# Kernel optimization log

Hardware: AMD Instinct MI355X
Metric: run time of the kernel (lower is better)

Reference implementation:

```python
import jax, jax.numpy as jnp
import numpy as np

N_HEADS = 16
WINDOW_SIZE = 128


def setup_inputs() -> dict:
    key = jax.random.key(0)
    ks = jax.random.split(key, 5)
    B, T, D = 2, 2048, 1024
    x = jax.random.normal(ks[0], (B, T, D), dtype=jnp.float32)
    w_qkv = jax.random.normal(ks[1], (3 * D, D), dtype=jnp.float32) * (D ** -0.5)
    b_qkv = jax.random.normal(ks[2], (3 * D,), dtype=jnp.float32) * 0.01
    w_out = jax.random.normal(ks[3], (D, D), dtype=jnp.float32) * (D ** -0.5)
    b_out = jax.random.normal(ks[4], (D,), dtype=jnp.float32) * 0.01
    return {"x": x, "w_qkv": w_qkv, "b_qkv": b_qkv, "w_out": w_out, "b_out": b_out}


def reference(x, w_qkv, b_qkv, w_out, b_out):
    B, T, D = x.shape
    H = N_HEADS
    hd = D // H
    scale = hd ** -0.5

    # qkv projection: (B,T,3D) -> (3,B,H,T,hd)
    qkv = (x @ w_qkv.T + b_qkv).reshape(B, T, 3, H, hd)
    qkv = jnp.transpose(qkv, (2, 0, 3, 1, 4))
    q, k, v = qkv[0], qkv[1], qkv[2]

    pos = jnp.arange(T)
    # mask[i, j]: |j - i| <= w/2 and j >= i  (faithful to original, which
    # due to its index orientation allows query i to attend to keys j >= i)
    mask = (jnp.abs(pos[None, :] - pos[:, None]) <= WINDOW_SIZE // 2) & (
        pos[None, :] >= pos[:, None]
    )

    attn = jnp.einsum("bhqd,bhkd->bhqk", q, k) * scale  # (B,H,T,T)
    attn = jnp.where(mask[None, None], attn, -jnp.inf)
    attn = jax.nn.softmax(attn, axis=-1)
    attn = jnp.nan_to_num(attn, nan=0.0)

    out = jnp.einsum("bhqk,bhkd->bhqd", attn, v)  # (B,H,T,hd)
    out = jnp.transpose(out, (0, 2, 1, 3)).reshape(B, T, D)
    return out @ w_out.T + b_out
```

## Files before the change

### kernel.cpp

```cpp
#include <hip/hip_runtime.h>
#include <hip/hip_bf16.h>
#include <stdint.h>


typedef short bf16x8 __attribute__((ext_vector_type(8)));
typedef float f32x4 __attribute__((ext_vector_type(4)));

typedef const __attribute__((address_space(1))) void* gptr_t;
typedef __attribute__((address_space(3))) void* lptr_t;

__device__ __forceinline__ float bf2f(short u) {
    union { float f; uint32_t i; } x;
    x.i = ((uint32_t)(uint16_t)u) << 16;
    return x.f;
}
__device__ __forceinline__ short f2bf(float f) {
    __hip_bfloat16 h = __float2bfloat16(f);
    return *reinterpret_cast<short*>(&h);
}

__global__ __launch_bounds__(256)
void convert_all(const float* __restrict__ x, const float* __restrict__ wq,
                 const float* __restrict__ bq, const float* __restrict__ wo,
                 const float* __restrict__ bo,
                 short* __restrict__ xb, short* __restrict__ wqb, short* __restrict__ bqb,
                 short* __restrict__ wob, short* __restrict__ bob) {
    int i = blockIdx.x * 256 + threadIdx.x;
    const float* src; short* dst; int o;
    if      (i <  524288) { src = x;  dst = xb;  o = i; }
    else if (i <  917504) { src = wq; dst = wqb; o = i - 524288; }
    else if (i <  917888) { src = bq; dst = bqb; o = i - 917504; }
    else if (i < 1048960) { src = wo; dst = wob; o = i - 917888; }
    else if (i < 1049088) { src = bo; dst = bob; o = i - 1048960; }
    else return;
    const int e = o * 8;
    float4 a = *(const float4*)(src + e);
    float4 b = *(const float4*)(src + e + 4);
    short t[8];
    t[0] = f2bf(a.x); t[1] = f2bf(a.y); t[2] = f2bf(a.z); t[3] = f2bf(a.w);
    t[4] = f2bf(b.x); t[5] = f2bf(b.y); t[6] = f2bf(b.z); t[7] = f2bf(b.w);
    *(uint4*)(dst + e) = *(const uint4*)t;
}

__global__ __launch_bounds__(256)
void gemm_bt_128(const short* __restrict__ A, const short* __restrict__ Bt,
                 const short* __restrict__ bias, short* __restrict__ C,
                 int M, int N, int K) {
    __shared__ short As[128 * 32];
    __shared__ short Bs[128 * 32];

    const int tid  = threadIdx.x;
    const int lane = tid & 63;
    const int w    = tid >> 6;
    const int qd   = lane >> 4;
    const int l16  = lane & 15;
    const int wm   = w >> 1;
    const int wn   = w & 1;
    const int mBase = blockIdx.y * 128;
    const int nBase = blockIdx.x * 128;

    f32x4 acc[4][4] = {};

    const int nK = K >> 5;
    for (int kt = 0; kt < nK; ++kt) {
        const int kb = kt << 5;
#pragma unroll
        for (int i = 0; i < 2; ++i) {
            const int e   = i * 2048 + tid * 8;
            const int row = e >> 5;
            const int col = e & 31;
            const short* ga = A  + (size_t)(mBase + row) * K + kb + col;
            const short* gb = Bt + (size_t)(nBase + row) * K + kb + col;
            lptr_t la = (lptr_t)(As + i * 2048 + w * 512);
            lptr_t lb = (lptr_t)(Bs + i * 2048 + w * 512);
            __builtin_amdgcn_global_load_lds((gptr_t)ga, la, 16, 0, 0);
            __builtin_amdgcn_global_load_lds((gptr_t)gb, lb, 16, 0, 0);
        }
        __syncthreads();

        bf16x8 af[4], bfr[4];
#pragma unroll
        for (int mi = 0; mi < 4; ++mi)
            af[mi] = *(const bf16x8*)(As + (wm * 64 + mi * 16 + l16) * 32 + qd * 8);
#pragma unroll
        for (int ni = 0; ni < 4; ++ni)
            bfr[ni] = *(const bf16x8*)(Bs + (wn * 64 + ni * 16 + l16) * 32 + qd * 8);
#pragma unroll
        for (int mi = 0; mi < 4; ++mi)
#pragma unroll
            for (int ni = 0; ni < 4; ++ni)
                acc[mi][ni] = __builtin_amdgcn_mfma_f32_16x16x32_bf16(
                    bfr[ni], af[mi], acc[mi][ni], 0, 0, 0);
        __syncthreads();
    }

#pragma unroll
    for (int ni = 0; ni < 4; ++ni) {
        const int n0 = nBase + wn * 64 + ni * 16 + qd * 4;
        float bv[4];
#pragma unroll
        for (int r = 0; r < 4; ++r) bv[r] = bf2f(bias[n0 + r]);
#pragma unroll
        for (int mi = 0; mi < 4; ++mi) {
            const int m = mBase + wm * 64 + mi * 16 + l16;
            short t[4];
#pragma unroll
            for (int r = 0; r < 4; ++r) t[r] = f2bf(acc[mi][ni][r] + bv[r]);
            *(uint2*)&C[(size_t)m * N + n0] = *(const uint2*)t;
        }
    }
}

__global__ __launch_bounds__(256)
void gemm_bt_64(const short* __restrict__ A, const short* __restrict__ Bt,
                const short* __restrict__ bias, float* __restrict__ C,
                int M, int N, int K) {
    __shared__ short As[64 * 32];
    __shared__ short Bs[128 * 32];

    const int tid  = threadIdx.x;
    const int lane = tid & 63;
    const int w    = tid >> 6;
    const int qd   = lane >> 4;
    const int l16  = lane & 15;
    const int wm   = w >> 1;
    const int wn   = w & 1;
    const int mBase = blockIdx.y * 64;
    const int nBase = blockIdx.x * 128;

    f32x4 acc[2][4] = {};

    const int nK = K >> 5;
    for (int kt = 0; kt < nK; ++kt) {
        const int kb = kt << 5;
        {
            const int e   = tid * 8;
            const int row = e >> 5;
            const int col = e & 31;
            const short* ga = A + (size_t)(mBase + row) * K + kb + col;
            lptr_t la = (lptr_t)(As + w * 512);
            __builtin_amdgcn_global_load_lds((gptr_t)ga, la, 16, 0, 0);
        }
#pragma unroll
        for (int i = 0; i < 2; ++i) {
            const int e   = i * 2048 + tid * 8;
            const int row = e >> 5;
            const int col = e & 31;
            const short* gb = Bt + (size_t)(nBase + row) * K + kb + col;
            lptr_t lb = (lptr_t)(Bs + i * 2048 + w * 512);
            __builtin_amdgcn_global_load_lds((gptr_t)gb, lb, 16, 0, 0);
        }
        __syncthreads();

        bf16x8 af[2], bfr[4];
#pragma unroll
        for (int mi = 0; mi < 2; ++mi)
            af[mi] = *(const bf16x8*)(As + (wm * 32 + mi * 16 + l16) * 32 + qd * 8);
#pragma unroll
        for (int ni = 0; ni < 4; ++ni)
            bfr[ni] = *(const bf16x8*)(Bs + (wn * 64 + ni * 16 + l16) * 32 + qd * 8);
#pragma unroll
        for (int mi = 0; mi < 2; ++mi)
#pragma unroll
            for (int ni = 0; ni < 4; ++ni)
                acc[mi][ni] = __builtin_amdgcn_mfma_f32_16x16x32_bf16(
                    bfr[ni], af[mi], acc[mi][ni], 0, 0, 0);
        __syncthreads();
    }

#pragma unroll
    for (int ni = 0; ni < 4; ++ni) {
        const int n0 = nBase + wn * 64 + ni * 16 + qd * 4;
        float bv[4];
#pragma unroll
        for (int r = 0; r < 4; ++r) bv[r] = bf2f(bias[n0 + r]);
#pragma unroll
        for (int mi = 0; mi < 2; ++mi) {
            const int m = mBase + wm * 32 + mi * 16 + l16;
            f32x4 o;
#pragma unroll
            for (int r = 0; r < 4; ++r) o[r] = acc[mi][ni][r] + bv[r];
            *(f32x4*)&C[(size_t)m * N + n0] = o;
        }
    }
}

__global__ __launch_bounds__(256)
void attn_mfma(const short* __restrict__ qkv, short* __restrict__ attn_out, int B, int T) {
    __shared__ short k_s[128 * 72];
    __shared__ short v_s[144 * 66];
    __shared__ short p_s[64 * 104];

    const int tid  = threadIdx.x;
    const int lane = tid & 63;
    const int w    = tid >> 6;
    const int qd   = lane >> 4;
    const int l16  = lane & 15;
    const int qs   = blockIdx.x * 64;
    const int h    = blockIdx.y;
    const int b    = blockIdx.z;
    const size_t rs   = 3072;
    const size_t base = (size_t)b * T * rs;
    const int qoff = h * 64, koff = 1024 + h * 64, voff = 2048 + h * 64;

#pragma unroll
    for (int i = 0; i < 5; ++i) {
        const int c   = tid + i * 256;
        const int row = c >> 3;
        if (row >= 144) break;
        const int ch = (c & 7) * 8;
        int gr = qs + row; if (gr > T - 1) gr = T - 1;
        uint4 uv = *(const uint4*)(qkv + base + (size_t)gr * rs + voff + ch);
        if (row < 128) {
            uint4 uk = *(const uint4*)(qkv + base + (size_t)gr * rs + koff + ch);
            *(uint4*)&k_s[row * 72 + ch] = uk;
        }
        const uint32_t* vp = (const uint32_t*)&uv;
        uint32_t* vd = (uint32_t*)&v_s[row * 66 + ch];
        vd[0] = vp[0]; vd[1] = vp[1]; vd[2] = vp[2]; vd[3] = vp[3];
    }
    __syncthreads();

    bf16x8 aq0, aq1;
    {
        const short* g = qkv + base + (size_t)(qs + 16 * w + l16) * rs + qoff + qd * 8;
        aq0 = *(const bf16x8*)(g);
        aq1 = *(const bf16x8*)(g + 32);
    }

    f32x4 sacc[5] = {};
#pragma unroll
    for (int u = 0; u < 5; ++u) {
        const int krow = 16 * (w + u) + l16;
        bf16x8 bk0 = *(const bf16x8*)&k_s[krow * 72 + qd * 8];
        bf16x8 bk1 = *(const bf16x8*)&k_s[krow * 72 + 32 + qd * 8];
        sacc[u] = __builtin_amdgcn_mfma_f32_16x16x32_bf16(aq0, bk0, sacc[u], 0, 0, 0);
        sacc[u] = __builtin_amdgcn_mfma_f32_16x16x32_bf16(aq1, bk1, sacc[u], 0, 0, 0);
    }

    const float scale = 0.125f;
    float pw[5][4];
    float inv[4];
#pragma unroll
    for (int r = 0; r < 4; ++r) {
        const int m = 4 * qd + r;
        float mx = -3.4e38f;
#pragma unroll
        for (int u = 0; u < 5; ++u) {
            const int rel = 16 * u + l16 - m;
            const int j   = qs + 16 * (w + u) + l16;
            const bool ok = (rel >= 0) & (rel <= 64) & (j < T);
            const float v = ok ? sacc[u][r] * scale : -3.4e38f;
            pw[u][r] = v;
            mx = fmaxf(mx, v);
        }
#pragma unroll
        for (int msk = 1; msk <= 8; msk <<= 1) mx = fmaxf(mx, __shfl_xor(mx, msk));
        float sum = 0.f;
#pragma unroll
        for (int u = 0; u < 5; ++u) {
            float e = (pw[u][r] <= -3.0e38f) ? 0.f : __expf(pw[u][r] - mx);
            pw[u][r] = e;
            sum += e;
        }
#pragma unroll
        for (int msk = 1; msk <= 8; msk <<= 1) sum += __shfl_xor(sum, msk);
        inv[r] = 1.0f / sum;
    }

#pragma unroll
    for (int u = 0; u < 5; ++u)
#pragma unroll
        for (int r = 0; r < 4; ++r)
            p_s[(16 * w + 4 * qd + r) * 104 + 16 * u + l16] = f2bf(pw[u][r] * inv[r]);
#pragma unroll
    for (int r = 0; r < 4; ++r)
        p_s[(16 * w + 4 * qd + r) * 104 + 80 + l16] = 0;

    f32x4 oacc[4] = {};
#pragma unroll
    for (int ks = 0; ks < 3; ++ks) {
        bf16x8 ap = *(const bf16x8*)&p_s[(16 * w + l16) * 104 + ks * 32 + qd * 8];
#pragma unroll
        for (int dt = 0; dt < 4; ++dt) {
            short t[8];
#pragma unroll
            for (int j = 0; j < 8; ++j)
                t[j] = v_s[(16 * w + ks * 32 + qd * 8 + j) * 66 + 16 * dt + l16];
            bf16x8 bv = *(const bf16x8*)t;
            oacc[dt] = __builtin_amdgcn_mfma_f32_16x16x32_bf16(bv, ap, oacc[dt], 0, 0, 0);
        }
    }

    const size_t row = (size_t)(b * T + qs + 16 * w + l16);
#pragma unroll
    for (int dt = 0; dt < 4; ++dt) {
        short t[4];
#pragma unroll
        for (int r = 0; r < 4; ++r) t[r] = f2bf(oacc[dt][r]);
        *(uint2*)&attn_out[row * 1024 + h * 64 + dt * 16 + qd * 4] = *(const uint2*)t;
    }
}

extern "C" void kernel_launch(void* const* d_in, const int* in_sizes, int n_in,
                              void* d_out, int out_size, void* d_ws, size_t ws_size,
                              hipStream_t stream) {
    (void)in_sizes; (void)n_in; (void)out_size; (void)ws_size;
    const int B = 2, T = 2048, D = 1024;
    const int M = B * T;

    char* ws = (char*)d_ws;
    size_t off = 0;
    short* xb   = (short*)(ws + off); off += (size_t)M * D * 2;
    short* wqkb = (short*)(ws + off); off += (size_t)3 * D * D * 2;
    short* bqkb = (short*)(ws + off); off += (size_t)3 * D * 2;
    short* wob  = (short*)(ws + off); off += (size_t)D * D * 2;
    short* bob  = (short*)(ws + off); off += (size_t)D * 2;
    short* qkv  = (short*)(ws + off); off += (size_t)M * 3 * D * 2;
    short* attn = (short*)(ws + off); off += (size_t)M * D * 2;

    convert_all<<<dim3(4099), 256, 0, stream>>>(
        (const float*)d_in[0], (const float*)d_in[1], (const float*)d_in[2],
        (const float*)d_in[3], (const float*)d_in[4], xb, wqkb, bqkb, wob, bob);

    gemm_bt_128<<<dim3(3 * D / 128, M / 128), 256, 0, stream>>>(
        xb, wqkb, bqkb, qkv, M, 3 * D, D);
    attn_mfma<<<dim3(T / 64, 16, B), 256, 0, stream>>>(qkv, attn, B, T);
    gemm_bt_64<<<dim3(D / 128, M / 64), 256, 0, stream>>>(
        attn, wob, bob, (float*)d_out, M, D, D);
}
```

Baseline: 164.5 us.

## Split-K output projection with a separate bias-reduce kernel and transposed MFMA epilogues

The output projection GEMM now splits K into two halves across blockIdx.z. Each half writes fp32 partials into workspace reused from the dead xb/qkv buffers, and a new reduce kernel adds the two partials plus the fp32 bias. The intent is to double the block count so the GPU is better filled. Both GEMMs also swap MFMA operand order, so the epilogue stores scalar elements with columns contiguous across lanes instead of vector stores. The cost is extra global traffic for the partials, one more kernel launch, and narrower stores.

```diff
diff --git a/kernel.cpp b/kernel.cpp
--- a/kernel.cpp
+++ b/kernel.cpp
@@ -43,9 +43,9 @@
 }
 
 __global__ __launch_bounds__(256)
-void gemm_bt_128(const short* __restrict__ A, const short* __restrict__ Bt,
-                 const short* __restrict__ bias, short* __restrict__ C,
-                 int M, int N, int K) {
+void gemm1_qkv(const short* __restrict__ A, const short* __restrict__ Bt,
+               const short* __restrict__ bias, short* __restrict__ C,
+               int M, int N, int K) {
     __shared__ short As[128 * 32];
     __shared__ short Bs[128 * 32];
 
@@ -90,31 +90,27 @@
 #pragma unroll
             for (int ni = 0; ni < 4; ++ni)
                 acc[mi][ni] = __builtin_amdgcn_mfma_f32_16x16x32_bf16(
-                    bfr[ni], af[mi], acc[mi][ni], 0, 0, 0);
+                    af[mi], bfr[ni], acc[mi][ni], 0, 0, 0);
         __syncthreads();
     }
 
 #pragma unroll
     for (int ni = 0; ni < 4; ++ni) {
-        const int n0 = nBase + wn * 64 + ni * 16 + qd * 4;
-        float bv[4];
-#pragma unroll
-        for (int r = 0; r < 4; ++r) bv[r] = bf2f(bias[n0 + r]);
-#pragma unroll
-        for (int mi = 0; mi < 4; ++mi) {
-            const int m = mBase + wm * 64 + mi * 16 + l16;
-            short t[4];
-#pragma unroll
-            for (int r = 0; r < 4; ++r) t[r] = f2bf(acc[mi][ni][r] + bv[r]);
-            *(uint2*)&C[(size_t)m * N + n0] = *(const uint2*)t;
-        }
-    }
-}
-
-__global__ __launch_bounds__(256)
-void gemm_bt_64(const short* __restrict__ A, const short* __restrict__ Bt,
-                const short* __restrict__ bias, float* __restrict__ C,
-                int M, int N, int K) {
+        const int n = nBase + wn * 64 + ni * 16 + l16;
+        const float bv = bf2f(bias[n]);
+#pragma unroll
+        for (int mi = 0; mi < 4; ++mi)
+#pragma unroll
+            for (int r = 0; r < 4; ++r) {
+                const int m = mBase + wm * 64 + mi * 16 + qd * 4 + r;
+                C[(size_t)m * N + n] = f2bf(acc[mi][ni][r] + bv);
+            }
+    }
+}
+
+__global__ __launch_bounds__(256)
+void gemm2_splitk(const short* __restrict__ A, const short* __restrict__ Bt,
+                  float* __restrict__ P, int M, int N, int K) {
     __shared__ short As[64 * 32];
     __shared__ short Bs[128 * 32];
 
@@ -127,12 +123,15 @@
     const int wn   = w & 1;
     const int mBase = blockIdx.y * 64;
     const int nBase = blockIdx.x * 128;
+    const int kz    = blockIdx.z;
 
     f32x4 acc[2][4] = {};
 
-    const int nK = K >> 5;
+    const int kHalf = K >> 1;
+    const int k0 = kz * kHalf;
+    const int nK = kHalf >> 5;
     for (int kt = 0; kt < nK; ++kt) {
-        const int kb = kt << 5;
+        const int kb = k0 + (kt << 5);
         {
             const int e   = tid * 8;
             const int row = e >> 5;
@@ -164,25 +163,38 @@
 #pragma unroll
             for (int ni = 0; ni < 4; ++ni)
                 acc[mi][ni] = __builtin_amdgcn_mfma_f32_16x16x32_bf16(
-                    bfr[ni], af[mi], acc[mi][ni], 0, 0, 0);
+                    af[mi], bfr[ni], acc[mi][ni], 0, 0, 0);
         __syncthreads();
     }
 
+    float* Pk = P + (size_t)kz * M * N;
 #pragma unroll
     for (int ni = 0; ni < 4; ++ni) {
-        const int n0 = nBase + wn * 64 + ni * 16 + qd * 4;
-        float bv[4];
-#pragma unroll
-        for (int r = 0; r < 4; ++r) bv[r] = bf2f(bias[n0 + r]);
-#pragma unroll
-        for (int mi = 0; mi < 2; ++mi) {
-            const int m = mBase + wm * 32 + mi * 16 + l16;
-            f32x4 o;
-#pragma unroll
-            for (int r = 0; r < 4; ++r) o[r] = acc[mi][ni][r] + bv[r];
-            *(f32x4*)&C[(size_t)m * N + n0] = o;
-        }
-    }
+        const int n = nBase + wn * 64 + ni * 16 + l16;
+#pragma unroll
+        for (int mi = 0; mi < 2; ++mi)
+#pragma unroll
+            for (int r = 0; r < 4; ++r) {
+                const int m = mBase + wm * 32 + mi * 16 + qd * 4 + r;
+                Pk[(size_t)m * N + n] = acc[mi][ni][r];
+            }
+    }
+}
+
+__global__ __launch_bounds__(256)
+void reduce_bias(const float* __restrict__ P, const float* __restrict__ bias,
+                 float* __restrict__ out, int MN, int N) {
+    const int e = (blockIdx.x * 256 + threadIdx.x) * 4;
+    if (e >= MN) return;
+    float4 a = *(const float4*)(P + e);
+    float4 b = *(const float4*)(P + MN + e);
+    float4 bv = *(const float4*)(bias + (e & (N - 1)));
+    float4 o;
+    o.x = a.x + b.x + bv.x;
+    o.y = a.y + b.y + bv.y;
+    o.z = a.z + b.z + bv.z;
+    o.w = a.w + b.w + bv.w;
+    *(float4*)(out + e) = o;
 }
 
 __global__ __launch_bounds__(256)
@@ -312,20 +324,23 @@
     char* ws = (char*)d_ws;
     size_t off = 0;
     short* xb   = (short*)(ws + off); off += (size_t)M * D * 2;
+    short* qkv  = (short*)(ws + off); off += (size_t)M * 3 * D * 2;
+    short* attn = (short*)(ws + off); off += (size_t)M * D * 2;
     short* wqkb = (short*)(ws + off); off += (size_t)3 * D * D * 2;
     short* bqkb = (short*)(ws + off); off += (size_t)3 * D * 2;
     short* wob  = (short*)(ws + off); off += (size_t)D * D * 2;
     short* bob  = (short*)(ws + off); off += (size_t)D * 2;
-    short* qkv  = (short*)(ws + off); off += (size_t)M * 3 * D * 2;
-    short* attn = (short*)(ws + off); off += (size_t)M * D * 2;
+    float* part = (float*)ws;
 
     convert_all<<<dim3(4099), 256, 0, stream>>>(
         (const float*)d_in[0], (const float*)d_in[1], (const float*)d_in[2],
         (const float*)d_in[3], (const float*)d_in[4], xb, wqkb, bqkb, wob, bob);
 
-    gemm_bt_128<<<dim3(3 * D / 128, M / 128), 256, 0, stream>>>(
+    gemm1_qkv<<<dim3(3 * D / 128, M / 128), 256, 0, stream>>>(
         xb, wqkb, bqkb, qkv, M, 3 * D, D);
     attn_mfma<<<dim3(T / 64, 16, B), 256, 0, stream>>>(qkv, attn, B, T);
-    gemm_bt_64<<<dim3(D / 128, M / 64), 256, 0, stream>>>(
-        attn, wob, bob, (float*)d_out, M, D, D);
-}
+    gemm2_splitk<<<dim3(D / 128, M / 64, 2), 256, 0, stream>>>(
+        attn, wob, part, M, D, D);
+    reduce_bias<<<dim3(M * D / 4 / 256), 256, 0, stream>>>(
+        part, (const float*)d_in[4], (float*)d_out, M * D, D);
+}
```

Result: no change. 165.8 us (+0.8%).
